# Kernel optimization log

Hardware: AMD Instinct MI355X
Metric: run time of the kernel (lower is better)

The kernel has to match this reference:

```python
import jax, jax.numpy as jnp
import numpy as np

P, B, FEAT, HID, ATTN, NHEAD = 4096, 32, 512, 512, 512, 8
HD = ATTN // NHEAD  # 64


def setup_inputs() -> dict:
    key = jax.random.key(0)
    ks = jax.random.split(key, 12)
    s = lambda n: 1.0 / np.sqrt(n)
    return {
        "last_hidden": jax.random.normal(ks[0], (1, B, HID), jnp.float32),
        "encoder_outputs": jax.random.normal(ks[1], (P, B, FEAT), jnp.float32),
        # outer projections (stored [in, out]; torch Linear is x @ W.T + b)
        "Wa_w": jax.random.uniform(ks[2], (FEAT, ATTN), jnp.float32, -s(FEAT), s(FEAT)),
        "Wa_b": jax.random.uniform(ks[3], (ATTN,), jnp.float32, -s(FEAT), s(FEAT)),
        "Ua_w": jax.random.uniform(ks[4], (HID, ATTN), jnp.float32, -s(HID), s(HID)),
        "Ua_b": jax.random.uniform(ks[5], (ATTN,), jnp.float32, -s(HID), s(HID)),
        # inner Attention(head_attn_size, head_attn_size, head_attn_size)
        "Wa2_w": jax.random.uniform(ks[6], (HD, HD), jnp.float32, -s(HD), s(HD)),
        "Wa2_b": jax.random.uniform(ks[7], (HD,), jnp.float32, -s(HD), s(HD)),
        "Ua2_w": jax.random.uniform(ks[8], (HD, HD), jnp.float32, -s(HD), s(HD)),
        "Ua2_b": jax.random.uniform(ks[9], (HD,), jnp.float32, -s(HD), s(HD)),
        "va_w": jax.random.uniform(ks[10], (HD, 1), jnp.float32, -s(HD), s(HD)),
        "va_b": jax.random.uniform(ks[11], (1,), jnp.float32, -s(HD), s(HD)),
        "nhead": NHEAD,
    }


def reference(last_hidden, encoder_outputs, Wa_w, Wa_b, Ua_w, Ua_b,
              Wa2_w, Wa2_b, Ua2_w, Ua2_b, va_w, va_b, nhead):
    p, b = encoder_outputs.shape[:2]
    enc = encoder_outputs @ Wa_w + Wa_b            # [P,B,A]
    hid = last_hidden @ Ua_w + Ua_b                # [1,B,A]
    hd = enc.shape[-1] // nhead
    enc = enc.reshape(p, b, nhead, hd)             # [P,B,nh,hd]
    hid = hid.reshape(1, b, nhead, hd)             # [1,B,nh,hd]
    # inner Bahdanau attention
    a = jnp.tanh((enc @ Wa2_w + Wa2_b) + (hid @ Ua2_w + Ua2_b))
    scores = a @ va_w + va_b                       # [P,B,nh,1]
    weights = jax.nn.softmax(scores, axis=0)       # softmax over pixels
    context = jnp.sum(weights * enc, axis=0, keepdims=True)  # [1,B,nh,hd]
    weight = jnp.mean(weights, axis=-2)            # mean over heads -> [P,B,1]
    context = context.reshape(1, b, nhead * hd)    # [1,B,A]
    return context, weight
```

## Files before the change

### kernel.cpp

```cpp
#include <hip/hip_runtime.h>
#include <hip/hip_bf16.h>

#define PDIM 4096
#define BDIM 32
#define MDIM (PDIM*BDIM)
#define KDIM 512
#define NDIM 512
#define NH   8
#define HD   64

typedef __attribute__((ext_vector_type(4))) float f32x4;
typedef __attribute__((ext_vector_type(8))) short bf16x8;

__device__ __forceinline__ unsigned short f2bf(float f) {
  unsigned u = __float_as_uint(f);
  u += 0x7fffu + ((u >> 16) & 1u);
  return (unsigned short)(u >> 16);
}
__device__ __forceinline__ float bf2f(unsigned short u) {
  return __uint_as_float(((unsigned)u) << 16);
}

__device__ __forceinline__ float fast_tanh(float x) {
  x = fminf(fmaxf(x, -15.f), 15.f);
  float e = __expf(2.f * x);
  return __fdividef(e - 1.f, e + 1.f);
}

#define GLOAD_LDS16(g, l) __builtin_amdgcn_global_load_lds( \
    (const __attribute__((address_space(1))) void*)(g),     \
    (__attribute__((address_space(3))) void*)(l), 16, 0, 0)

__global__ __launch_bounds__(256) void cvt_k(
    const float* __restrict__ x, unsigned short* __restrict__ xbf) {
  size_t i = ((size_t)blockIdx.x * 256 + threadIdx.x) * 8;
  float4 a = *(const float4*)(x + i);
  float4 b = *(const float4*)(x + i + 4);
  ushort4 o0; o0.x = f2bf(a.x); o0.y = f2bf(a.y); o0.z = f2bf(a.z); o0.w = f2bf(a.w);
  ushort4 o1; o1.x = f2bf(b.x); o1.y = f2bf(b.y); o1.z = f2bf(b.z); o1.w = f2bf(b.w);
  *(ushort4*)(xbf + i) = o0;
  *(ushort4*)(xbf + i + 4) = o1;
}

__global__ __launch_bounds__(512) void hub_k(
    const float* __restrict__ lh, const float* __restrict__ Ua,
    const float* __restrict__ Ua_b, const float* __restrict__ Ua2,
    const float* __restrict__ Ua2_b, const float* __restrict__ Wa_b,
    const float* __restrict__ Wa2, const float* __restrict__ Wa2_b,
    float* __restrict__ ubf) {
  int b = blockIdx.x, tid = threadIdx.x;
  __shared__ float ls[512];
  __shared__ float hs[512];
  ls[tid] = lh[b*512 + tid];
  __syncthreads();
  float s = Ua_b[tid];
  #pragma unroll 8
  for (int k = 0; k < 512; ++k)
    s += ls[k] * Ua[(size_t)k*512 + tid];
  hs[tid] = s;
  __syncthreads();
  int h = tid >> 6, j = tid & 63;
  float u = Ua2_b[j] + Wa2_b[j];
  #pragma unroll 4
  for (int k = 0; k < 64; ++k) {
    u += hs[h*64 + k] * Ua2[k*64 + j];
    u += Wa_b[h*64 + k] * Wa2[k*64 + j];
  }
  ubf[b*512 + tid] = u;
}

__global__ __launch_bounds__(256) void wft_k(
    const float* __restrict__ Wa, const float* __restrict__ Wa2,
    unsigned short* __restrict__ WfT) {
  int n = blockIdx.x, tid = threadIdx.x;
  int h = n >> 6, j = n & 63;
  __shared__ float w2[64];
  if (tid < 64) w2[tid] = Wa2[tid*64 + j];
  __syncthreads();
  for (int k = tid; k < 512; k += 256) {
    float s = 0.f;
    #pragma unroll 8
    for (int kk = 0; kk < 64; ++kk)
      s += Wa[(size_t)k*512 + h*64 + kk] * w2[kk];
    WfT[(size_t)n*512 + k] = f2bf(s);
  }
}

__global__ __launch_bounds__(256, 4) void gemm_score_k(
    const unsigned short* __restrict__ xbf, const unsigned short* __restrict__ WfT,
    const float* __restrict__ ubf, const float* __restrict__ va_w,
    const float* __restrict__ va_b, float* __restrict__ scores) {
  __shared__ __align__(16) unsigned short sm[16384];
  unsigned short* As = sm;
  unsigned short* Bs = sm + 8192;
  int tid = threadIdx.x;
  int orig = blockIdx.x;
  int wg = (orig & 7) * 512 + (orig >> 3);
  int bn = wg & 3, bm = wg >> 2;
  int m0 = bm*128, n0 = bn*128;
  int lane = tid & 63, w = tid >> 6;
  int quad = lane >> 4, l16 = lane & 15;
  int wr = w >> 1, wc = w & 1;
  f32x4 acc[4][4] = {};

  for (int k0 = 0; k0 < KDIM; k0 += 64) {
    __syncthreads();
    #pragma unroll
    for (int i = 0; i < 4; ++i) {
      int c = i*256 + tid;
      int r = c & 127, kc = c >> 7;
      GLOAD_LDS16(xbf + (size_t)(m0 + r)*512 + k0 + kc*8, As + (size_t)c*8);
    }
    #pragma unroll
    for (int i = 0; i < 4; ++i) {
      int c = i*256 + tid;
      int r = c & 127, kc = c >> 7;
      GLOAD_LDS16(WfT + (size_t)(n0 + r)*512 + k0 + kc*8, Bs + (size_t)c*8);
    }
    __syncthreads();
    #pragma unroll
    for (int kk = 0; kk < 64; kk += 32) {
      int kc = (kk >> 3) + quad;
      bf16x8 af[4], bfr[4];
      #pragma unroll
      for (int ti = 0; ti < 4; ++ti)
        af[ti] = *(const bf16x8*)(As + ((size_t)kc*128 + 64*wr + 16*ti + l16)*8);
      #pragma unroll
      for (int tj = 0; tj < 4; ++tj)
        bfr[tj] = *(const bf16x8*)(Bs + ((size_t)kc*128 + 64*wc + 16*tj + l16)*8);
      #pragma unroll
      for (int ti = 0; ti < 4; ++ti)
        #pragma unroll
        for (int tj = 0; tj < 4; ++tj)
          acc[ti][tj] = __builtin_amdgcn_mfma_f32_16x16x32_bf16(
              af[ti], bfr[tj], acc[ti][tj], 0, 0, 0);
    }
  }

  __syncthreads();
  float* ubf_s = (float*)sm;
  #pragma unroll
  for (int t = 0; t < 16; ++t) {
    int idx = t*256 + tid;
    int b = idx >> 7, c = idx & 127;
    ubf_s[b*129 + c] = ubf[b*512 + n0 + c];
  }
  __syncthreads();

  int head = bn*2 + wc;
  float va_r[4];
  #pragma unroll
  for (int tj = 0; tj < 4; ++tj) va_r[tj] = va_w[16*tj + l16];
  float vb = va_b[0];
  #pragma unroll
  for (int ti = 0; ti < 4; ++ti) {
    #pragma unroll
    for (int r = 0; r < 4; ++r) {
      int row_loc = 64*wr + 16*ti + 4*quad + r;
      int b31 = row_loc & 31;
      float s = 0.f;
      #pragma unroll
      for (int tj = 0; tj < 4; ++tj) {
        float xa = acc[ti][tj][r] + ubf_s[b31*129 + 64*wc + 16*tj + l16];
        s += fast_tanh(xa) * va_r[tj];
      }
      s += __shfl_xor(s, 1); s += __shfl_xor(s, 2);
      s += __shfl_xor(s, 4); s += __shfl_xor(s, 8);
      if (l16 == 0) {
        int m = m0 + row_loc;
        scores[((size_t)head*32 + (m & 31))*4096 + (m >> 5)] = s + vb;
      }
    }
  }
}

__global__ __launch_bounds__(256) void softmax_k(
    const float* __restrict__ sc, float* __restrict__ w) {
  int bh = blockIdx.x;
  int tid = threadIdx.x;
  const float* row = sc + (size_t)bh*4096;
  float4 v[4];
  float mx = -1e30f;
  #pragma unroll
  for (int i = 0; i < 4; ++i) {
    v[i] = *(const float4*)(row + (size_t)(i*256 + tid)*4);
    mx = fmaxf(mx, fmaxf(fmaxf(v[i].x, v[i].y), fmaxf(v[i].z, v[i].w)));
  }
  #pragma unroll
  for (int m = 1; m < 64; m <<= 1) mx = fmaxf(mx, __shfl_xor(mx, m));
  __shared__ float redm[4], reds[4];
  int wid = tid >> 6, lane = tid & 63;
  if (lane == 0) redm[wid] = mx;
  __syncthreads();
  mx = fmaxf(fmaxf(redm[0], redm[1]), fmaxf(redm[2], redm[3]));
  float sum = 0.f;
  #pragma unroll
  for (int i = 0; i < 4; ++i) {
    v[i].x = __expf(v[i].x - mx); v[i].y = __expf(v[i].y - mx);
    v[i].z = __expf(v[i].z - mx); v[i].w = __expf(v[i].w - mx);
    sum += v[i].x + v[i].y + v[i].z + v[i].w;
  }
  #pragma unroll
  for (int m = 1; m < 64; m <<= 1) sum += __shfl_xor(sum, m);
  if (lane == 0) reds[wid] = sum;
  __syncthreads();
  sum = reds[0] + reds[1] + reds[2] + reds[3];
  float inv = 1.f / sum;
  float* dst = w + (size_t)bh*4096;
  #pragma unroll
  for (int i = 0; i < 4; ++i) {
    float4 o; o.x = v[i].x*inv; o.y = v[i].y*inv; o.z = v[i].z*inv; o.w = v[i].w*inv;
    *(float4*)(dst + (size_t)(i*256 + tid)*4) = o;
  }
}

__global__ __launch_bounds__(256) void mean_k(
    const float* __restrict__ w, float* __restrict__ out) {
  int p0 = blockIdx.x * 256;
  int tid = threadIdx.x;
  float s[32];
  #pragma unroll
  for (int b = 0; b < 32; ++b) s[b] = 0.f;
  for (int h = 0; h < 8; ++h) {
    #pragma unroll
    for (int b = 0; b < 32; ++b)
      s[b] += w[((size_t)h*32 + b)*4096 + p0 + tid];
  }
  float4* dst = (float4*)(out + BDIM*NDIM + (size_t)(p0 + tid)*32);
  #pragma unroll
  for (int j = 0; j < 8; ++j) {
    float4 o;
    o.x = s[4*j]*0.125f; o.y = s[4*j+1]*0.125f;
    o.z = s[4*j+2]*0.125f; o.w = s[4*j+3]*0.125f;
    dst[j] = o;
  }
}

__global__ __launch_bounds__(256) void ctx_partial_k(
    const unsigned short* __restrict__ xbf, const float* __restrict__ w,
    float* __restrict__ part) {
  int pc = blockIdx.x;
  int b  = blockIdx.y;
  int tid = threadIdx.x;
  __shared__ float wl[8*256];
  __shared__ float red[4][512];
  #pragma unroll
  for (int h = 0; h < 8; ++h)
    wl[h*256 + tid] = w[((size_t)h*32 + b)*4096 + pc*256 + tid];
  __syncthreads();
  int lane = tid & 63, wv = tid >> 6;
  float acc[8][8];
  #pragma unroll
  for (int h = 0; h < 8; ++h)
    #pragma unroll
    for (int j = 0; j < 8; ++j) acc[h][j] = 0.f;
  for (int i = 0; i < 64; ++i) {
    int pl = wv*64 + i;
    bf16x8 xv = *(const bf16x8*)(xbf + ((size_t)((pc*256 + pl)*32 + b))*512 + lane*8);
    float xf[8];
    #pragma unroll
    for (int j = 0; j < 8; ++j) xf[j] = bf2f((unsigned short)xv[j]);
    #pragma unroll
    for (int h = 0; h < 8; ++h) {
      float ww = wl[h*256 + pl];
      #pragma unroll
      for (int j = 0; j < 8; ++j) acc[h][j] += ww * xf[j];
    }
  }
  for (int h = 0; h < 8; ++h) {
    #pragma unroll
    for (int j = 0; j < 8; j += 4)
      *(float4*)(&red[wv][lane*8 + j]) = *(float4*)(&acc[h][j]);
    __syncthreads();
    if (tid < 64) {
      #pragma unroll
      for (int j = 0; j < 8; ++j) {
        int f = tid*8 + j;
        part[((size_t)(b*16 + pc)*NH + h)*512 + f] =
            red[0][f] + red[1][f] + red[2][f] + red[3][f];
      }
    }
    __syncthreads();
  }
}

__global__ __launch_bounds__(256) void ctx_reduce_k(
    const float* __restrict__ part, float* __restrict__ cx) {
  int gid = blockIdx.x*256 + threadIdx.x;
  float s = 0.f;
  int f = gid & 511;
  int bh = gid >> 9;
  int h = bh & 7, b = bh >> 3;
  #pragma unroll
  for (int pc = 0; pc < 16; ++pc)
    s += part[((size_t)(b*16 + pc)*NH + h)*512 + f];
  cx[gid] = s;
}

__global__ __launch_bounds__(256) void ctx_proj_k(
    const float* __restrict__ cx, const float* __restrict__ Wa,
    const float* __restrict__ Wa_b, float* __restrict__ out) {
  int b = blockIdx.x >> 3, h = blockIdx.x & 7;
  int tid = threadIdx.x;
  __shared__ float cs[512];
  cs[tid]       = cx[(size_t)blockIdx.x*512 + tid];
  cs[tid + 256] = cx[(size_t)blockIdx.x*512 + tid + 256];
  __syncthreads();
  int d = tid & 63, g = tid >> 6;
  float s = 0.f;
  #pragma unroll 8
  for (int f = g*128; f < g*128 + 128; ++f)
    s += cs[f] * Wa[(size_t)f*512 + h*64 + d];
  __shared__ float red[256];
  red[tid] = s;
  __syncthreads();
  if (tid < 64) {
    float tot = red[tid] + red[64+tid] + red[128+tid] + red[192+tid] + Wa_b[h*64 + tid];
    out[b*512 + h*64 + tid] = tot;
  }
}

extern "C" void kernel_launch(void* const* d_in, const int* in_sizes, int n_in,
                              void* d_out, int out_size, void* d_ws, size_t ws_size,
                              hipStream_t stream) {
  (void)in_sizes; (void)n_in; (void)out_size; (void)ws_size;
  const float* lh    = (const float*)d_in[0];
  const float* x     = (const float*)d_in[1];
  const float* Wa_w  = (const float*)d_in[2];
  const float* Wa_b  = (const float*)d_in[3];
  const float* Ua_w  = (const float*)d_in[4];
  const float* Ua_b  = (const float*)d_in[5];
  const float* Wa2_w = (const float*)d_in[6];
  const float* Wa2_b = (const float*)d_in[7];
  const float* Ua2_w = (const float*)d_in[8];
  const float* Ua2_b = (const float*)d_in[9];
  const float* va_w  = (const float*)d_in[10];
  const float* va_b  = (const float*)d_in[11];
  float* out = (float*)d_out;
  char* ws = (char*)d_ws;

  unsigned short* xbf = (unsigned short*)(ws);
  unsigned short* WfT = (unsigned short*)(ws + 134217728);
  float* ubf    = (float*)(ws + 134742016);
  float* scores = (float*)(ws + 134807552);
  float* w      = (float*)(ws + 139001856);
  float* part   = (float*)(ws + 143196160);
  float* cx     = (float*)(ws + 151584768);

  hipLaunchKernelGGL(cvt_k, dim3(32768), dim3(256), 0, stream, x, xbf);
  hipLaunchKernelGGL(hub_k, dim3(32), dim3(512), 0, stream,
                     lh, Ua_w, Ua_b, Ua2_w, Ua2_b, Wa_b, Wa2_w, Wa2_b, ubf);
  hipLaunchKernelGGL(wft_k, dim3(512), dim3(256), 0, stream, Wa_w, Wa2_w, WfT);
  hipLaunchKernelGGL(gemm_score_k, dim3(4096), dim3(256), 0, stream,
                     xbf, WfT, ubf, va_w, va_b, scores);
  hipLaunchKernelGGL(softmax_k, dim3(256), dim3(256), 0, stream, scores, w);
  hipLaunchKernelGGL(mean_k, dim3(16), dim3(256), 0, stream, w, out);
  hipLaunchKernelGGL(ctx_partial_k, dim3(16, 32), dim3(256), 0, stream, xbf, w, part);
  hipLaunchKernelGGL(ctx_reduce_k, dim3(512), dim3(256), 0, stream, part, cx);
  hipLaunchKernelGGL(ctx_proj_k, dim3(256), dim3(256), 0, stream, cx, Wa_w, Wa_b, out);
}
```

Measured before the change: 643.6 us.

## Triple-buffer GEMM K-loop with async global-to-LDS prefetch and MFMA priority

Restructures the bf16 GEMM main loop into a 3-stage ring of 32-wide K tiles. Loads for tile t+2 are issued while tile t is computed, using vmcnt waits and a single barrier per step instead of two syncthreads per 64-wide tile. s_setprio is raised around the MFMA block. The LDS footprint grows to 48KB and launch bounds drop to 3 blocks per CU, so occupancy is traded for overlap of memory and compute.

```diff
diff --git a/kernel.cpp b/kernel.cpp
--- a/kernel.cpp
+++ b/kernel.cpp
@@ -86,13 +86,11 @@
   }
 }
 
-__global__ __launch_bounds__(256, 4) void gemm_score_k(
+__global__ __launch_bounds__(256, 3) void gemm_score_k(
     const unsigned short* __restrict__ xbf, const unsigned short* __restrict__ WfT,
     const float* __restrict__ ubf, const float* __restrict__ va_w,
     const float* __restrict__ va_b, float* __restrict__ scores) {
-  __shared__ __align__(16) unsigned short sm[16384];
-  unsigned short* As = sm;
-  unsigned short* Bs = sm + 8192;
+  __shared__ __align__(16) unsigned short sm[3*8192];
   int tid = threadIdx.x;
   int orig = blockIdx.x;
   int wg = (orig & 7) * 512 + (orig >> 3);
@@ -103,38 +101,50 @@
   int wr = w >> 1, wc = w & 1;
   f32x4 acc[4][4] = {};
 
-  for (int k0 = 0; k0 < KDIM; k0 += 64) {
-    __syncthreads();
-    #pragma unroll
-    for (int i = 0; i < 4; ++i) {
+  auto STAGE = [&](int u, int s) {
+    unsigned short* As = sm + s*8192;
+    unsigned short* Bs = sm + s*8192 + 4096;
+    int k0 = u*32;
+    #pragma unroll
+    for (int i = 0; i < 2; ++i) {
       int c = i*256 + tid;
       int r = c & 127, kc = c >> 7;
       GLOAD_LDS16(xbf + (size_t)(m0 + r)*512 + k0 + kc*8, As + (size_t)c*8);
     }
     #pragma unroll
-    for (int i = 0; i < 4; ++i) {
+    for (int i = 0; i < 2; ++i) {
       int c = i*256 + tid;
       int r = c & 127, kc = c >> 7;
       GLOAD_LDS16(WfT + (size_t)(n0 + r)*512 + k0 + kc*8, Bs + (size_t)c*8);
     }
-    __syncthreads();
-    #pragma unroll
-    for (int kk = 0; kk < 64; kk += 32) {
-      int kc = (kk >> 3) + quad;
-      bf16x8 af[4], bfr[4];
-      #pragma unroll
-      for (int ti = 0; ti < 4; ++ti)
-        af[ti] = *(const bf16x8*)(As + ((size_t)kc*128 + 64*wr + 16*ti + l16)*8);
+  };
+
+  STAGE(0, 0);
+  STAGE(1, 1);
+
+  #pragma unroll
+  for (int t = 0; t < 16; ++t) {
+    if (t == 15) asm volatile("s_waitcnt vmcnt(0)" ::: "memory");
+    else         asm volatile("s_waitcnt vmcnt(4)" ::: "memory");
+    __builtin_amdgcn_s_barrier();
+    if (t + 2 < 16) STAGE(t + 2, (t + 2) % 3);
+    const unsigned short* As = sm + (t % 3)*8192;
+    const unsigned short* Bs = As + 4096;
+    bf16x8 af[4], bfr[4];
+    #pragma unroll
+    for (int ti = 0; ti < 4; ++ti)
+      af[ti] = *(const bf16x8*)(As + ((size_t)quad*128 + 64*wr + 16*ti + l16)*8);
+    #pragma unroll
+    for (int tj = 0; tj < 4; ++tj)
+      bfr[tj] = *(const bf16x8*)(Bs + ((size_t)quad*128 + 64*wc + 16*tj + l16)*8);
+    __builtin_amdgcn_s_setprio(1);
+    #pragma unroll
+    for (int ti = 0; ti < 4; ++ti)
       #pragma unroll
       for (int tj = 0; tj < 4; ++tj)
-        bfr[tj] = *(const bf16x8*)(Bs + ((size_t)kc*128 + 64*wc + 16*tj + l16)*8);
-      #pragma unroll
-      for (int ti = 0; ti < 4; ++ti)
-        #pragma unroll
-        for (int tj = 0; tj < 4; ++tj)
-          acc[ti][tj] = __builtin_amdgcn_mfma_f32_16x16x32_bf16(
-              af[ti], bfr[tj], acc[ti][tj], 0, 0, 0);
-    }
+        acc[ti][tj] = __builtin_amdgcn_mfma_f32_16x16x32_bf16(
+            af[ti], bfr[tj], acc[ti][tj], 0, 0, 0);
+    __builtin_amdgcn_s_setprio(0);
   }
 
   __syncthreads();
```

Result: no change. 647.1 us (+0.6%).
